# Kernel optimization log

Measured on AMD Instinct MI355X. Metric: run time of the kernel, lower is better.

Reference implementation:

```python
import jax, jax.numpy as jnp
import numpy as np

EPS = 1e-5


def conv3d(x, w, b, stride, pad, groups):
    # x: [B,C,D,H,W], w: [O, C//groups, kd, kh, kw]
    out = jax.lax.conv_general_dilated(
        x, w, (stride, stride, stride), [(pad, pad)] * 3,
        dimension_numbers=("NCDHW", "OIDHW", "NCDHW"),
        feature_group_count=groups)
    return out + b[None, :, None, None, None]


def setup_inputs() -> dict:
    key = jax.random.key(0)
    ks = jax.random.split(key, 8)
    B, N, C, h = 4, 4096, 256, 8
    s = lambda k, shp, sc=0.02: jax.random.normal(k, shp, jnp.float32) * sc
    return {
        "x": jax.random.normal(ks[0], (B, N, C), jnp.float32),
        "q_dw_w": s(ks[1], (C, 1, 3, 3, 3)), "q_dw_b": jnp.zeros((C,), jnp.float32),
        "bn_gamma": jnp.ones((C,), jnp.float32), "bn_beta": jnp.zeros((C,), jnp.float32),
        "bn_mean": jnp.zeros((C,), jnp.float32), "bn_var": jnp.ones((C,), jnp.float32),
        "q_pw_w": s(ks[2], (C, C)), "q_pw_b": jnp.zeros((C,), jnp.float32),
        "sr_w": s(ks[3], (C, 1, 3, 3, 3)), "sr_b": jnp.zeros((C,), jnp.float32),
        "ln_gamma": jnp.ones((C,), jnp.float32), "ln_beta": jnp.zeros((C,), jnp.float32),
        "kv_w": s(ks[4], (2 * C, C)),
        "trans_w": s(ks[5], (h, h), 0.3), "trans_b": jnp.zeros((h,), jnp.float32),
        "proj_w": s(ks[6], (C, C)), "proj_b": jnp.zeros((C,), jnp.float32),
        "H": 16, "W": 16, "L": 16,
    }


def reference(x, q_dw_w, q_dw_b, bn_gamma, bn_beta, bn_mean, bn_var,
              q_pw_w, q_pw_b, sr_w, sr_b, ln_gamma, ln_beta, kv_w,
              trans_w, trans_b, proj_w, proj_b, H, W, L):
    B, N, C = x.shape
    h = trans_w.shape[0]
    d = C // h
    scale = d ** -0.5

    # [B,N,C] -> [B,C,H,W,L] (N split row-major into H,W,L)
    xq = x.reshape(B, H, W, L, C).transpose(0, 4, 1, 2, 3)

    # --- q path: SepConv3d = depthwise conv -> BatchNorm (inference) -> pointwise ---
    q = conv3d(xq, q_dw_w, q_dw_b, 1, 1, C)
    q = (q - bn_mean[None, :, None, None, None]) * (
        bn_gamma / jnp.sqrt(bn_var + EPS))[None, :, None, None, None] \
        + bn_beta[None, :, None, None, None]
    q = jnp.einsum("oc,bcxyz->boxyz", q_pw_w, q) + q_pw_b[None, :, None, None, None]
    # 'b (h d) l w k -> b h (lwk) d'
    q = q.reshape(B, h, d, N).transpose(0, 1, 3, 2)  # [B,h,N,d]

    # --- sr path: strided depthwise conv -> LayerNorm -> kv Linear ---
    xs = conv3d(xq, sr_w, sr_b, 2, 1, C)           # [B,C,H/2,W/2,L/2]
    M = xs.shape[2] * xs.shape[3] * xs.shape[4]
    xs = xs.reshape(B, C, M).transpose(0, 2, 1)     # [B,M,C]
    mu = xs.mean(-1, keepdims=True)
    var = xs.var(-1, keepdims=True)
    xs = (xs - mu) / jnp.sqrt(var + EPS) * ln_gamma + ln_beta
    kv = xs @ kv_w.T                                # [B,M,2C]
    kv = kv.reshape(B, M, 2, h, d).transpose(2, 0, 3, 1, 4)
    k, v = kv[0], kv[1]                             # [B,h,M,d]

    # --- attention with per-head 1x1 conv transform + InstanceNorm ---
    attn = jnp.einsum("bhnd,bhmd->bhnm", q, k) * scale      # [B,h,N,M]
    attn = jnp.einsum("ij,bjnm->binm", trans_w, attn) + trans_b[None, :, None, None]
    attn = jax.nn.softmax(attn, axis=-1)
    m2 = attn.mean((2, 3), keepdims=True)
    v2 = attn.var((2, 3), keepdims=True)
    attn = (attn - m2) / jnp.sqrt(v2 + EPS)

    out = jnp.einsum("bhnm,bhmd->bhnd", attn, v)
    out = out.transpose(0, 2, 1, 3).reshape(B, N, C)
    out = out @ proj_w.T + proj_b
    return out
```

## Files before the change

kernel.cpp:

```cpp
#include <hip/hip_runtime.h>
#include <hip/hip_bf16.h>

#define SCALE_QK 0.17677669529663687f

__global__ __launch_bounds__(256) void prep_kernel(
    const float* __restrict__ pw, const float* __restrict__ kvw,
    const float* __restrict__ pjw,
    float* __restrict__ wtpw, float* __restrict__ wtkv, float* __restrict__ wtpj,
    float* __restrict__ ssq, float* __restrict__ sumv) {
  const int g = blockIdx.x * 256 + threadIdx.x;
  if (g < 65536) {
    const int c = g >> 8, o = g & 255;
    wtpw[g] = pw[o * 256 + c];
  } else if (g < 196608) {
    const int g2 = g - 65536;
    const int c = g2 >> 9, o = g2 & 511;
    wtkv[g2] = kvw[o * 256 + c];
  } else {
    const int g3 = g - 196608;
    const int c = g3 >> 8, o = g3 & 255;
    wtpj[g3] = pjw[o * 256 + c];
  }
  if (g < 512) ssq[g] = 0.0f;
  if (g >= 512 && g < 512 + 1024) sumv[g - 512] = 0.0f;
}

__global__ __launch_bounds__(256) void dwbn_kernel(
    const float* __restrict__ x, const float* __restrict__ w,
    const float* __restrict__ wb, const float* __restrict__ bg,
    const float* __restrict__ bb, const float* __restrict__ bm,
    const float* __restrict__ bv, float* __restrict__ outq) {
  const int blk = blockIdx.x;
  const int b = blk >> 12, n = blk & 4095;
  const int i0 = n >> 8, i1 = (n >> 4) & 15, i2 = n & 15;
  const int c = threadIdx.x;
  float acc = wb[c];
#pragma unroll
  for (int k0 = 0; k0 < 3; ++k0) {
    const int z = i0 + k0 - 1;
    if ((unsigned)z >= 16u) continue;
#pragma unroll
    for (int k1 = 0; k1 < 3; ++k1) {
      const int y = i1 + k1 - 1;
      if ((unsigned)y >= 16u) continue;
#pragma unroll
      for (int k2 = 0; k2 < 3; ++k2) {
        const int xx = i2 + k2 - 1;
        if ((unsigned)xx >= 16u) continue;
        acc = fmaf(w[c * 27 + (k0 * 3 + k1) * 3 + k2],
                   x[((b * 4096) + ((z * 16 + y) * 16 + xx)) * 256 + c], acc);
      }
    }
  }
  const float sc = bg[c] * rsqrtf(bv[c] + 1e-5f);
  outq[blk * 256 + c] = (acc - bm[c]) * sc + bb[c];
}

__global__ __launch_bounds__(256) void srln_kernel(
    const float* __restrict__ x, const float* __restrict__ w,
    const float* __restrict__ wb, const float* __restrict__ lg,
    const float* __restrict__ lb, float* __restrict__ outx) {
  const int blk = blockIdx.x;
  const int b = blk >> 9, m = blk & 511;
  const int o0 = m >> 6, o1 = (m >> 3) & 7, o2 = m & 7;
  const int c = threadIdx.x;
  float acc = wb[c];
#pragma unroll
  for (int k0 = 0; k0 < 3; ++k0) {
    const int z = o0 * 2 + k0 - 1;
    if ((unsigned)z >= 16u) continue;
#pragma unroll
    for (int k1 = 0; k1 < 3; ++k1) {
      const int y = o1 * 2 + k1 - 1;
      if ((unsigned)y >= 16u) continue;
#pragma unroll
      for (int k2 = 0; k2 < 3; ++k2) {
        const int xx = o2 * 2 + k2 - 1;
        if ((unsigned)xx >= 16u) continue;
        acc = fmaf(w[c * 27 + (k0 * 3 + k1) * 3 + k2],
                   x[((b * 4096) + ((z * 16 + y) * 16 + xx)) * 256 + c], acc);
      }
    }
  }
  __shared__ float r1[4], r2[4];
  float s1 = acc, s2 = acc * acc;
#pragma unroll
  for (int off = 32; off >= 1; off >>= 1) {
    s1 += __shfl_xor(s1, off);
    s2 += __shfl_xor(s2, off);
  }
  const int t = threadIdx.x;
  if ((t & 63) == 0) { r1[t >> 6] = s1; r2[t >> 6] = s2; }
  __syncthreads();
  const float mu = (r1[0] + r1[1] + r1[2] + r1[3]) * (1.0f / 256.0f);
  const float ms = (r2[0] + r2[1] + r2[2] + r2[3]) * (1.0f / 256.0f);
  const float rs = rsqrtf(ms - mu * mu + 1e-5f);
  outx[blk * 256 + c] = (acc - mu) * rs * lg[c] + lb[c];
}

template <int MODE>
__global__ __launch_bounds__(256) void gemm_kernel(
    const float* __restrict__ A, const float* __restrict__ Wt,
    const float* __restrict__ bias, float* __restrict__ Out, const int ldW,
    const float* __restrict__ sumv, const float* __restrict__ rstd) {
  __shared__ float a_t[32][68];
  __shared__ float w_s[32][132];
  const int t = threadIdx.x;
  const int r0 = blockIdx.x * 64;
  const int c0 = blockIdx.y * 128;
  const int rt = t & 15, ct = t >> 4;
  const int bidx = r0 >> 12;
  const float invM = 1.0f / 512.0f;
  float acc[4][8];
#pragma unroll
  for (int rr = 0; rr < 4; ++rr)
#pragma unroll
    for (int cc = 0; cc < 8; ++cc) acc[rr][cc] = 0.0f;

  for (int k0 = 0; k0 < 256; k0 += 32) {
    {
      const int kk = t & 31;
      int rl = t >> 5;
#pragma unroll
      for (int p = 0; p < 8; ++p, rl += 8) {
        float v = A[(r0 + rl) * 256 + k0 + kk];
        if (MODE == 1) {
          const int kg = k0 + kk;
          v = (v - invM * sumv[bidx * 256 + kg]) * rstd[bidx * 8 + (kg >> 5)];
        }
        a_t[kk][rl] = v;
      }
    }
    {
      const int cq = (t & 31) * 4;
      int kk = t >> 5;
#pragma unroll
      for (int p = 0; p < 4; ++p, kk += 8) {
        const float4 v = *(const float4*)&Wt[(k0 + kk) * ldW + c0 + cq];
        *(float4*)&w_s[kk][cq] = v;
      }
    }
    __syncthreads();
#pragma unroll
    for (int kk = 0; kk < 32; ++kk) {
      const float4 a4 = *(const float4*)&a_t[kk][rt * 4];
      const float av[4] = {a4.x, a4.y, a4.z, a4.w};
      float4 w4[2];
#pragma unroll
      for (int q = 0; q < 2; ++q) w4[q] = *(const float4*)&w_s[kk][ct * 8 + q * 4];
#pragma unroll
      for (int rr = 0; rr < 4; ++rr) {
#pragma unroll
        for (int q = 0; q < 2; ++q) {
          acc[rr][q * 4 + 0] = fmaf(av[rr], w4[q].x, acc[rr][q * 4 + 0]);
          acc[rr][q * 4 + 1] = fmaf(av[rr], w4[q].y, acc[rr][q * 4 + 1]);
          acc[rr][q * 4 + 2] = fmaf(av[rr], w4[q].z, acc[rr][q * 4 + 2]);
          acc[rr][q * 4 + 3] = fmaf(av[rr], w4[q].w, acc[rr][q * 4 + 3]);
        }
      }
    }
    __syncthreads();
  }
#pragma unroll
  for (int rr = 0; rr < 4; ++rr) {
    const int row = r0 + rt * 4 + rr;
#pragma unroll
    for (int q = 0; q < 2; ++q) {
      const int cc = c0 + ct * 8 + q * 4;
      float4 o;
      o.x = acc[rr][q * 4 + 0];
      o.y = acc[rr][q * 4 + 1];
      o.z = acc[rr][q * 4 + 2];
      o.w = acc[rr][q * 4 + 3];
      if (bias != nullptr) {
        o.x += bias[cc + 0]; o.y += bias[cc + 1];
        o.z += bias[cc + 2]; o.w += bias[cc + 3];
      }
      *(float4*)&Out[row * ldW + cc] = o;
    }
  }
}

__global__ __launch_bounds__(256) void kt_kernel(const float* __restrict__ kvb,
                                                 float* __restrict__ ktb) {
  __shared__ float tile[32][33];
  const int blk = blockIdx.x;
  const int b = blk >> 7, mt = (blk >> 3) & 15, k8 = blk & 7;
  const int m0 = mt * 32, k0 = k8 * 32;
  const int t = threadIdx.x;
  {
    const int ml = t >> 3, kl = (t & 7) * 4;
    const float4 v = *(const float4*)&kvb[((b * 512 + m0 + ml) * 512) + k0 + kl];
    tile[ml][kl + 0] = v.x; tile[ml][kl + 1] = v.y;
    tile[ml][kl + 2] = v.z; tile[ml][kl + 3] = v.w;
  }
  __syncthreads();
  {
    const int kl = t >> 3, ml = (t & 7) * 4;
    float4 o;
    o.x = tile[ml + 0][kl]; o.y = tile[ml + 1][kl];
    o.z = tile[ml + 2][kl]; o.w = tile[ml + 3][kl];
    *(float4*)&ktb[((b * 256 + k0 + kl) * 512) + m0 + ml] = o;
  }
}

__global__ __launch_bounds__(256) void sumv_kernel(const float* __restrict__ kvb,
                                                   float* __restrict__ sumv) {
  const int blk = blockIdx.x;
  const int b = blk >> 3, grp = blk & 7;
  const int c = threadIdx.x;
  float s = 0.0f;
  for (int mm = 0; mm < 64; ++mm) {
    const int m = grp * 64 + mm;
    s += kvb[((b * 512 + m) * 512) + 256 + c];
  }
  atomicAdd(&sumv[b * 256 + c], s);
}

__global__ void rstd_kernel(const float* __restrict__ ssq, float* __restrict__ rstd) {
  const int t = threadIdx.x;
  if (t < 32) {
    float s = 0.0f;
#pragma unroll
    for (int sp = 0; sp < 16; ++sp) s += ssq[sp * 32 + t];
    const float e2 = s * (1.0f / (4096.0f * 512.0f));
    const float invM = 1.0f / 512.0f;
    rstd[t] = rsqrtf(e2 - invM * invM + 1e-5f);
  }
}

__device__ __forceinline__ int pswz2(int row, int m) {
  const int q = m >> 2;
  const int qs = q ^ ((q >> 3) & 7);
  return row * 512 + (qs << 2) + (m & 3);
}

__global__ __launch_bounds__(512, 4) void attn_kernel(
    const float* __restrict__ qb, const float* __restrict__ ktb,
    const float* __restrict__ kvb, const float* __restrict__ tw,
    float* __restrict__ ssq, float* __restrict__ out_un) {
  __shared__ float P[16384];
  __shared__ float Qs[8 * 256];
  __shared__ float sq_lds[8][8];
  const int t = threadIdx.x;
  const int blk = blockIdx.x;
  const int b = blk >> 9;
  const int n0 = (blk & 511) << 3;
  const int w = t >> 6, l = t & 63;

  {
    const int row = t >> 6, kq = t & 63;
    const float4 v = *(const float4*)&qb[((b * 4096 + n0 + row) * 256) + kq * 4];
    float4 s;
    s.x = v.x * SCALE_QK; s.y = v.y * SCALE_QK;
    s.z = v.z * SCALE_QK; s.w = v.w * SCALE_QK;
    *(float4*)&Qs[row * 256 + kq * 4] = s;
  }
  __syncthreads();

  float acc[8][8];
#pragma unroll
  for (int r = 0; r < 8; ++r)
#pragma unroll
    for (int e = 0; e < 8; ++e) acc[r][e] = 0.0f;
  {
    const float* ktr = &ktb[(size_t)((b * 256 + w * 32) << 9)];
    const int m2 = l * 2;
#pragma unroll 4
    for (int k = 0; k < 32; ++k) {
      const float2 c0 = *(const float2*)&ktr[(k << 9) + m2];
      const float2 c1 = *(const float2*)&ktr[(k << 9) + 128 + m2];
      const float2 c2 = *(const float2*)&ktr[(k << 9) + 256 + m2];
      const float2 c3 = *(const float2*)&ktr[(k << 9) + 384 + m2];
#pragma unroll
      for (int r = 0; r < 8; ++r) {
        const float qv = Qs[r * 256 + w * 32 + k];
        acc[r][0] = fmaf(qv, c0.x, acc[r][0]); acc[r][1] = fmaf(qv, c0.y, acc[r][1]);
        acc[r][2] = fmaf(qv, c1.x, acc[r][2]); acc[r][3] = fmaf(qv, c1.y, acc[r][3]);
        acc[r][4] = fmaf(qv, c2.x, acc[r][4]); acc[r][5] = fmaf(qv, c2.y, acc[r][5]);
        acc[r][6] = fmaf(qv, c3.x, acc[r][6]); acc[r][7] = fmaf(qv, c3.y, acc[r][7]);
      }
    }
  }

  float Wr[8][8];
#pragma unroll
  for (int i = 0; i < 8; ++i)
#pragma unroll
    for (int jj = 0; jj < 8; ++jj) Wr[i][jj] = tw[i * 8 + jj];

  float mixed[8][8];
#pragma unroll
  for (int i = 0; i < 8; ++i)
#pragma unroll
    for (int e = 0; e < 8; ++e) mixed[i][e] = 0.0f;

#pragma unroll
  for (int r = 0; r < 8; ++r) {
    float2 s0; s0.x = acc[r][0]; s0.y = acc[r][1];
    float2 s1; s1.x = acc[r][2]; s1.y = acc[r][3];
    *(float2*)&P[(r * 8 + w) * 256 + l * 2] = s0;
    *(float2*)&P[(r * 8 + w) * 256 + 128 + l * 2] = s1;
  }
  __syncthreads();
#pragma unroll
  for (int jj = 0; jj < 8; ++jj) {
    const float2 ra = *(const float2*)&P[(w * 8 + jj) * 256 + l * 2];
    const float2 rb = *(const float2*)&P[(w * 8 + jj) * 256 + 128 + l * 2];
#pragma unroll
    for (int i = 0; i < 8; ++i) {
      mixed[i][0] = fmaf(Wr[i][jj], ra.x, mixed[i][0]);
      mixed[i][1] = fmaf(Wr[i][jj], ra.y, mixed[i][1]);
      mixed[i][2] = fmaf(Wr[i][jj], rb.x, mixed[i][2]);
      mixed[i][3] = fmaf(Wr[i][jj], rb.y, mixed[i][3]);
    }
  }
  __syncthreads();
#pragma unroll
  for (int r = 0; r < 8; ++r) {
    float2 s0; s0.x = acc[r][4]; s0.y = acc[r][5];
    float2 s1; s1.x = acc[r][6]; s1.y = acc[r][7];
    *(float2*)&P[(r * 8 + w) * 256 + l * 2] = s0;
    *(float2*)&P[(r * 8 + w) * 256 + 128 + l * 2] = s1;
  }
  __syncthreads();
#pragma unroll
  for (int jj = 0; jj < 8; ++jj) {
    const float2 ra = *(const float2*)&P[(w * 8 + jj) * 256 + l * 2];
    const float2 rb = *(const float2*)&P[(w * 8 + jj) * 256 + 128 + l * 2];
#pragma unroll
    for (int i = 0; i < 8; ++i) {
      mixed[i][4] = fmaf(Wr[i][jj], ra.x, mixed[i][4]);
      mixed[i][5] = fmaf(Wr[i][jj], ra.y, mixed[i][5]);
      mixed[i][6] = fmaf(Wr[i][jj], rb.x, mixed[i][6]);
      mixed[i][7] = fmaf(Wr[i][jj], rb.y, mixed[i][7]);
    }
  }
  __syncthreads();

#pragma unroll
  for (int i = 0; i < 8; ++i) {
    float mx = mixed[i][0];
#pragma unroll
    for (int e = 1; e < 8; ++e) mx = fmaxf(mx, mixed[i][e]);
#pragma unroll
    for (int off = 32; off >= 1; off >>= 1) mx = fmaxf(mx, __shfl_xor(mx, off));
    float s = 0.0f;
#pragma unroll
    for (int e = 0; e < 8; ++e) {
      const float ev = __expf(mixed[i][e] - mx);
      mixed[i][e] = ev;
      s += ev;
    }
#pragma unroll
    for (int off = 32; off >= 1; off >>= 1) s += __shfl_xor(s, off);
    const float rinv = 1.0f / s;
    float sq = 0.0f;
#pragma unroll
    for (int e = 0; e < 8; ++e) {
      const float p = mixed[i][e] * rinv;
      mixed[i][e] = p;
      sq = fmaf(p, p, sq);
    }
#pragma unroll
    for (int off = 32; off >= 1; off >>= 1) sq += __shfl_xor(sq, off);
    if (l == 0) sq_lds[w][i] = sq;
  }
  __syncthreads();
  if (t < 8) {
    float s8 = 0.0f;
#pragma unroll
    for (int r = 0; r < 8; ++r) s8 += sq_lds[r][t];
    atomicAdd(&ssq[(blk & 15) * 32 + b * 8 + t], s8);
  }

  const int il = w & 3, mh = w >> 2;
  const int mgrp = l >> 3, dl = l & 7;

#pragma unroll
  for (int i = 0; i < 4; ++i) {
#pragma unroll
    for (int e = 0; e < 4; ++e) {
      float2 pv;
      pv.x = mixed[i][e * 2 + 0];
      pv.y = mixed[i][e * 2 + 1];
      *(float2*)&P[pswz2(w * 4 + i, e * 128 + l * 2)] = pv;
    }
  }
  __syncthreads();
  {
    float av[8][4];
#pragma unroll
    for (int r = 0; r < 8; ++r)
#pragma unroll
      for (int e = 0; e < 4; ++e) av[r][e] = 0.0f;
    const int mb = mh * 256 + mgrp * 32;
    const int vcol = 256 + il * 32 + dl * 4;
#pragma unroll 2
    for (int mq = 0; mq < 8; ++mq) {
      const int m0 = mb + mq * 4;
      float4 p4[8];
#pragma unroll
      for (int r = 0; r < 8; ++r) p4[r] = *(const float4*)&P[pswz2(r * 4 + il, m0)];
#pragma unroll
      for (int e = 0; e < 4; ++e) {
        const float4 v4 = *(const float4*)&kvb[((b * 512 + m0 + e) * 512) + vcol];
#pragma unroll
        for (int r = 0; r < 8; ++r) {
          const float p = (&p4[r].x)[e];
          av[r][0] = fmaf(p, v4.x, av[r][0]);
          av[r][1] = fmaf(p, v4.y, av[r][1]);
          av[r][2] = fmaf(p, v4.z, av[r][2]);
          av[r][3] = fmaf(p, v4.w, av[r][3]);
        }
      }
    }
#pragma unroll
    for (int r = 0; r < 8; ++r)
#pragma unroll
      for (int e = 0; e < 4; ++e) {
        float v = av[r][e];
        v += __shfl_xor(v, 8);
        v += __shfl_xor(v, 16);
        v += __shfl_xor(v, 32);
        av[r][e] = v;
      }
    __syncthreads();
    if (l < 8) {
#pragma unroll
      for (int r = 0; r < 8; ++r) {
        float4 o;
        o.x = av[r][0]; o.y = av[r][1]; o.z = av[r][2]; o.w = av[r][3];
        *(float4*)&P[w * 256 + r * 32 + dl * 4] = o;
      }
    }
  }
  __syncthreads();
#pragma unroll
  for (int rep = 0; rep < 2; ++rep) {
    const int idx = rep * 512 + t;
    const int il2 = idx >> 8, r2i = (idx >> 5) & 7, dd = idx & 31;
    const float s = P[il2 * 256 + r2i * 32 + dd] + P[(il2 + 4) * 256 + r2i * 32 + dd];
    out_un[((b * 4096) + n0 + r2i) * 256 + il2 * 32 + dd] = s;
  }
  __syncthreads();

#pragma unroll
  for (int i = 0; i < 4; ++i) {
#pragma unroll
    for (int e = 0; e < 4; ++e) {
      float2 pv;
      pv.x = mixed[4 + i][e * 2 + 0];
      pv.y = mixed[4 + i][e * 2 + 1];
      *(float2*)&P[pswz2(w * 4 + i, e * 128 + l * 2)] = pv;
    }
  }
  __syncthreads();
  {
    float av[8][4];
#pragma unroll
    for (int r = 0; r < 8; ++r)
#pragma unroll
      for (int e = 0; e < 4; ++e) av[r][e] = 0.0f;
    const int mb = mh * 256 + mgrp * 32;
    const int vcol = 256 + (4 + il) * 32 + dl * 4;
#pragma unroll 2
    for (int mq = 0; mq < 8; ++mq) {
      const int m0 = mb + mq * 4;
      float4 p4[8];
#pragma unroll
      for (int r = 0; r < 8; ++r) p4[r] = *(const float4*)&P[pswz2(r * 4 + il, m0)];
#pragma unroll
      for (int e = 0; e < 4; ++e) {
        const float4 v4 = *(const float4*)&kvb[((b * 512 + m0 + e) * 512) + vcol];
#pragma unroll
        for (int r = 0; r < 8; ++r) {
          const float p = (&p4[r].x)[e];
          av[r][0] = fmaf(p, v4.x, av[r][0]);
          av[r][1] = fmaf(p, v4.y, av[r][1]);
          av[r][2] = fmaf(p, v4.z, av[r][2]);
          av[r][3] = fmaf(p, v4.w, av[r][3]);
        }
      }
    }
#pragma unroll
    for (int r = 0; r < 8; ++r)
#pragma unroll
      for (int e = 0; e < 4; ++e) {
        float v = av[r][e];
        v += __shfl_xor(v, 8);
        v += __shfl_xor(v, 16);
        v += __shfl_xor(v, 32);
        av[r][e] = v;
      }
    __syncthreads();
    if (l < 8) {
#pragma unroll
      for (int r = 0; r < 8; ++r) {
        float4 o;
        o.x = av[r][0]; o.y = av[r][1]; o.z = av[r][2]; o.w = av[r][3];
        *(float4*)&P[w * 256 + r * 32 + dl * 4] = o;
      }
    }
  }
  __syncthreads();
#pragma unroll
  for (int rep = 0; rep < 2; ++rep) {
    const int idx = rep * 512 + t;
    const int il2 = idx >> 8, r2i = (idx >> 5) & 7, dd = idx & 31;
    const float s = P[il2 * 256 + r2i * 32 + dd] + P[(il2 + 4) * 256 + r2i * 32 + dd];
    out_un[((b * 4096) + n0 + r2i) * 256 + (4 + il2) * 32 + dd] = s;
  }
}

extern "C" void kernel_launch(void* const* d_in, const int* in_sizes, int n_in,
                              void* d_out, int out_size, void* d_ws, size_t ws_size,
                              hipStream_t stream) {
  const float* x   = (const float*)d_in[0];
  const float* qdww= (const float*)d_in[1];
  const float* qdwb= (const float*)d_in[2];
  const float* bng = (const float*)d_in[3];
  const float* bnb = (const float*)d_in[4];
  const float* bnm = (const float*)d_in[5];
  const float* bnv = (const float*)d_in[6];
  const float* pw  = (const float*)d_in[7];
  const float* pwb = (const float*)d_in[8];
  const float* srw = (const float*)d_in[9];
  const float* srb = (const float*)d_in[10];
  const float* lng = (const float*)d_in[11];
  const float* lnb = (const float*)d_in[12];
  const float* kvw = (const float*)d_in[13];
  const float* tw  = (const float*)d_in[14];
  const float* pjw = (const float*)d_in[16];
  const float* pjb = (const float*)d_in[17];
  float* out = (float*)d_out;
  float* ws = (float*)d_ws;

  float* qdw   = ws + 0;
  float* qbuf  = ws + 4194304;
  float* xsln  = ws + 8388608;
  float* kvb   = ws + 8912896;
  float* ktb   = ws + 9961472;
  float* wtpw  = ws + 10485760;
  float* wtkv  = ws + 10551296;
  float* wtpj  = ws + 10682368;
  float* sumvp = ws + 10747904;
  float* ssqp  = ws + 10748928;
  float* rstdp = ws + 10749440;

  prep_kernel<<<1024, 256, 0, stream>>>(pw, kvw, pjw, wtpw, wtkv, wtpj, ssqp, sumvp);
  dwbn_kernel<<<16384, 256, 0, stream>>>(x, qdww, qdwb, bng, bnb, bnm, bnv, qdw);
  gemm_kernel<0><<<dim3(256, 2), 256, 0, stream>>>(qdw, wtpw, pwb, qbuf, 256, nullptr, nullptr);
  srln_kernel<<<2048, 256, 0, stream>>>(x, srw, srb, lng, lnb, xsln);
  gemm_kernel<0><<<dim3(32, 4), 256, 0, stream>>>(xsln, wtkv, nullptr, kvb, 512, nullptr, nullptr);
  kt_kernel<<<512, 256, 0, stream>>>(kvb, ktb);
  sumv_kernel<<<32, 256, 0, stream>>>(kvb, sumvp);
  attn_kernel<<<2048, 512, 0, stream>>>(qbuf, ktb, kvb, tw, ssqp, out);
  rstd_kernel<<<1, 64, 0, stream>>>(ssqp, rstdp);
  gemm_kernel<1><<<dim3(256, 2), 256, 0, stream>>>(out, wtpj, pjb, out, 256, sumvp, rstdp);
}
```

Baseline: 470.6 us.

## Compute QK scores with split-bf16 MFMA and fold head-mix into Q

```diff
diff --git a/kernel.cpp b/kernel.cpp
--- a/kernel.cpp
+++ b/kernel.cpp
@@ -2,6 +2,18 @@
 #include <hip/hip_bf16.h>
 
 #define SCALE_QK 0.17677669529663687f
+
+typedef __attribute__((ext_vector_type(8))) short bf16x8;
+typedef __attribute__((ext_vector_type(4))) float f32x4;
+
+__device__ __forceinline__ unsigned short bf16_rne(float v) {
+  const unsigned int b = __float_as_uint(v);
+  const unsigned int r = b + 0x7FFFu + ((b >> 16) & 1u);
+  return (unsigned short)(r >> 16);
+}
+__device__ __forceinline__ float bf16_f32(unsigned short h) {
+  return __uint_as_float(((unsigned int)h) << 16);
+}
 
 __global__ __launch_bounds__(256) void prep_kernel(
     const float* __restrict__ pw, const float* __restrict__ kvw,
@@ -182,7 +194,7 @@
 }
 
 __global__ __launch_bounds__(256) void kt_kernel(const float* __restrict__ kvb,
-                                                 float* __restrict__ ktb) {
+                                                 unsigned short* __restrict__ kthl) {
   __shared__ float tile[32][33];
   const int blk = blockIdx.x;
   const int b = blk >> 7, mt = (blk >> 3) & 15, k8 = blk & 7;
@@ -196,11 +208,27 @@
   }
   __syncthreads();
   {
-    const int kl = t >> 3, ml = (t & 7) * 4;
-    float4 o;
-    o.x = tile[ml + 0][kl]; o.y = tile[ml + 1][kl];
-    o.z = tile[ml + 2][kl]; o.w = tile[ml + 3][kl];
-    *(float4*)&ktb[((b * 256 + k0 + kl) * 512) + m0 + ml] = o;
+    const int s = t >> 7, kt8l = (t >> 5) & 3, mloc = t & 31;
+    unsigned int pk[4];
+#pragma unroll
+    for (int ep = 0; ep < 4; ++ep) {
+      unsigned short h0, h1;
+      {
+        const float v = tile[mloc][kt8l * 8 + ep * 2];
+        const unsigned short hi = bf16_rne(v);
+        h0 = (s == 0) ? hi : bf16_rne(v - bf16_f32(hi));
+      }
+      {
+        const float v = tile[mloc][kt8l * 8 + ep * 2 + 1];
+        const unsigned short hi = bf16_rne(v);
+        h1 = (s == 0) ? hi : bf16_rne(v - bf16_f32(hi));
+      }
+      pk[ep] = (unsigned int)h0 | ((unsigned int)h1 << 16);
+    }
+    const int kt8 = k8 * 4 + kt8l;
+    uint4 u;
+    u.x = pk[0]; u.y = pk[1]; u.z = pk[2]; u.w = pk[3];
+    *(uint4*)&kthl[((((size_t)b * 32 + kt8) * 512 + (m0 + mloc)) * 2 + s) * 8] = u;
   }
 }
 
@@ -236,141 +264,149 @@
 }
 
 __global__ __launch_bounds__(512, 4) void attn_kernel(
-    const float* __restrict__ qb, const float* __restrict__ ktb,
+    const float* __restrict__ qb, const unsigned short* __restrict__ kthl,
     const float* __restrict__ kvb, const float* __restrict__ tw,
     float* __restrict__ ssq, float* __restrict__ out_un) {
   __shared__ float P[16384];
-  __shared__ float Qs[8 * 256];
-  __shared__ float sq_lds[8][8];
-  const int t = threadIdx.x;
-  const int blk = blockIdx.x;
-  const int b = blk >> 9;
-  const int n0 = (blk & 511) << 3;
+  __shared__ float red[64][8][2];
+  __shared__ float red2[64][2];
+  __shared__ float sq_lds[64][8];
+  const int t = threadIdx.x, blk = blockIdx.x;
+  const int b = blk >> 9, n0 = (blk & 511) << 3;
   const int w = t >> 6, l = t & 63;
+  const int l15 = l & 15, l4 = l >> 4;
+  unsigned short* Au = (unsigned short*)P;
 
   {
-    const int row = t >> 6, kq = t & 63;
-    const float4 v = *(const float4*)&qb[((b * 4096 + n0 + row) * 256) + kq * 4];
-    float4 s;
-    s.x = v.x * SCALE_QK; s.y = v.y * SCALE_QK;
-    s.z = v.z * SCALE_QK; s.w = v.w * SCALE_QK;
-    *(float4*)&Qs[row * 256 + kq * 4] = s;
-  }
-  __syncthreads();
-
-  float acc[8][8];
-#pragma unroll
-  for (int r = 0; r < 8; ++r)
-#pragma unroll
-    for (int e = 0; e < 8; ++e) acc[r][e] = 0.0f;
-  {
-    const float* ktr = &ktb[(size_t)((b * 256 + w * 32) << 9)];
-    const int m2 = l * 2;
-#pragma unroll 4
-    for (int k = 0; k < 32; ++k) {
-      const float2 c0 = *(const float2*)&ktr[(k << 9) + m2];
-      const float2 c1 = *(const float2*)&ktr[(k << 9) + 128 + m2];
-      const float2 c2 = *(const float2*)&ktr[(k << 9) + 256 + m2];
-      const float2 c3 = *(const float2*)&ktr[(k << 9) + 384 + m2];
-#pragma unroll
-      for (int r = 0; r < 8; ++r) {
-        const float qv = Qs[r * 256 + w * 32 + k];
-        acc[r][0] = fmaf(qv, c0.x, acc[r][0]); acc[r][1] = fmaf(qv, c0.y, acc[r][1]);
-        acc[r][2] = fmaf(qv, c1.x, acc[r][2]); acc[r][3] = fmaf(qv, c1.y, acc[r][3]);
-        acc[r][4] = fmaf(qv, c2.x, acc[r][4]); acc[r][5] = fmaf(qv, c2.y, acc[r][5]);
-        acc[r][6] = fmaf(qv, c3.x, acc[r][6]); acc[r][7] = fmaf(qv, c3.y, acc[r][7]);
-      }
-    }
-  }
-
-  float Wr[8][8];
-#pragma unroll
-  for (int i = 0; i < 8; ++i)
-#pragma unroll
-    for (int jj = 0; jj < 8; ++jj) Wr[i][jj] = tw[i * 8 + jj];
-
-  float mixed[8][8];
-#pragma unroll
-  for (int i = 0; i < 8; ++i)
-#pragma unroll
-    for (int e = 0; e < 8; ++e) mixed[i][e] = 0.0f;
-
-#pragma unroll
-  for (int r = 0; r < 8; ++r) {
-    float2 s0; s0.x = acc[r][0]; s0.y = acc[r][1];
-    float2 s1; s1.x = acc[r][2]; s1.y = acc[r][3];
-    *(float2*)&P[(r * 8 + w) * 256 + l * 2] = s0;
-    *(float2*)&P[(r * 8 + w) * 256 + 128 + l * 2] = s1;
-  }
-  __syncthreads();
-#pragma unroll
-  for (int jj = 0; jj < 8; ++jj) {
-    const float2 ra = *(const float2*)&P[(w * 8 + jj) * 256 + l * 2];
-    const float2 rb = *(const float2*)&P[(w * 8 + jj) * 256 + 128 + l * 2];
+    const int r = t >> 6, c4 = (t & 63) * 4;
+    const float4 q4 = *(const float4*)&qb[((b * 4096 + n0 + r) * 256) + c4];
+    const float qv[4] = {q4.x, q4.y, q4.z, q4.w};
+    const int kt = c4 >> 5;
 #pragma unroll
     for (int i = 0; i < 8; ++i) {
-      mixed[i][0] = fmaf(Wr[i][jj], ra.x, mixed[i][0]);
-      mixed[i][1] = fmaf(Wr[i][jj], ra.y, mixed[i][1]);
-      mixed[i][2] = fmaf(Wr[i][jj], rb.x, mixed[i][2]);
-      mixed[i][3] = fmaf(Wr[i][jj], rb.y, mixed[i][3]);
-    }
-  }
-  __syncthreads();
-#pragma unroll
-  for (int r = 0; r < 8; ++r) {
-    float2 s0; s0.x = acc[r][4]; s0.y = acc[r][5];
-    float2 s1; s1.x = acc[r][6]; s1.y = acc[r][7];
-    *(float2*)&P[(r * 8 + w) * 256 + l * 2] = s0;
-    *(float2*)&P[(r * 8 + w) * 256 + 128 + l * 2] = s1;
-  }
-  __syncthreads();
-#pragma unroll
-  for (int jj = 0; jj < 8; ++jj) {
-    const float2 ra = *(const float2*)&P[(w * 8 + jj) * 256 + l * 2];
-    const float2 rb = *(const float2*)&P[(w * 8 + jj) * 256 + 128 + l * 2];
-#pragma unroll
-    for (int i = 0; i < 8; ++i) {
-      mixed[i][4] = fmaf(Wr[i][jj], ra.x, mixed[i][4]);
-      mixed[i][5] = fmaf(Wr[i][jj], ra.y, mixed[i][5]);
-      mixed[i][6] = fmaf(Wr[i][jj], rb.x, mixed[i][6]);
-      mixed[i][7] = fmaf(Wr[i][jj], rb.y, mixed[i][7]);
-    }
-  }
-  __syncthreads();
-
-#pragma unroll
-  for (int i = 0; i < 8; ++i) {
-    float mx = mixed[i][0];
-#pragma unroll
-    for (int e = 1; e < 8; ++e) mx = fmaxf(mx, mixed[i][e]);
-#pragma unroll
-    for (int off = 32; off >= 1; off >>= 1) mx = fmaxf(mx, __shfl_xor(mx, off));
-    float s = 0.0f;
-#pragma unroll
-    for (int e = 0; e < 8; ++e) {
-      const float ev = __expf(mixed[i][e] - mx);
-      mixed[i][e] = ev;
-      s += ev;
-    }
-#pragma unroll
-    for (int off = 32; off >= 1; off >>= 1) s += __shfl_xor(s, off);
-    const float rinv = 1.0f / s;
-    float sq = 0.0f;
-#pragma unroll
-    for (int e = 0; e < 8; ++e) {
-      const float p = mixed[i][e] * rinv;
-      mixed[i][e] = p;
-      sq = fmaf(p, p, sq);
-    }
-#pragma unroll
-    for (int off = 32; off >= 1; off >>= 1) sq += __shfl_xor(sq, off);
-    if (l == 0) sq_lds[w][i] = sq;
+      const float wij = tw[i * 8 + kt] * SCALE_QK;
+      const int mt = i >> 1;
+      const int rowin = (i & 1) * 8 + r;
+#pragma unroll
+      for (int cc = 0; cc < 4; ++cc) {
+        const int c = c4 + cc;
+        const float v = qv[cc] * wij;
+        const unsigned short hi = bf16_rne(v);
+        const unsigned short lo = bf16_rne(v - bf16_f32(hi));
+        const int lane = rowin | (((c & 31) >> 3) << 4);
+        const int idx = (((mt * 8 + kt) * 2) * 64 + lane) * 8 + (c & 7);
+        Au[idx] = hi;
+        Au[idx + 512] = lo;
+      }
+    }
+  }
+  __syncthreads();
+
+  f32x4 C[4][4];
+#pragma unroll
+  for (int mt = 0; mt < 4; ++mt)
+#pragma unroll
+    for (int tt = 0; tt < 4; ++tt) C[mt][tt] = (f32x4){0.f, 0.f, 0.f, 0.f};
+
+#pragma unroll
+  for (int kt = 0; kt < 8; ++kt) {
+#pragma unroll
+    for (int th = 0; th < 2; ++th) {
+      bf16x8 Bh[2], Bl[2];
+#pragma unroll
+      for (int tp = 0; tp < 2; ++tp) {
+        const int m = w * 64 + (th * 2 + tp) * 16 + l15;
+        const size_t bi = ((((size_t)b * 32 + kt * 4 + l4) * 512 + m) * 2) * 8;
+        Bh[tp] = *(const bf16x8*)&kthl[bi];
+        Bl[tp] = *(const bf16x8*)&kthl[bi + 8];
+      }
+#pragma unroll
+      for (int mt = 0; mt < 4; ++mt) {
+        const int ab = (((mt * 8 + kt) * 2) * 64 + l) * 8;
+        const bf16x8 Ah = *(const bf16x8*)&Au[ab];
+        const bf16x8 Al = *(const bf16x8*)&Au[ab + 512];
+#pragma unroll
+        for (int tp = 0; tp < 2; ++tp) {
+          const int ti = th * 2 + tp;
+          C[mt][ti] = __builtin_amdgcn_mfma_f32_16x16x32_bf16(Ah, Bh[tp], C[mt][ti], 0, 0, 0);
+          C[mt][ti] = __builtin_amdgcn_mfma_f32_16x16x32_bf16(Ah, Bl[tp], C[mt][ti], 0, 0, 0);
+          C[mt][ti] = __builtin_amdgcn_mfma_f32_16x16x32_bf16(Al, Bh[tp], C[mt][ti], 0, 0, 0);
+        }
+      }
+    }
+  }
+
+  float mxloc[4][4];
+#pragma unroll
+  for (int mt = 0; mt < 4; ++mt) {
+#pragma unroll
+    for (int rg = 0; rg < 4; ++rg) {
+      float mx = fmaxf(fmaxf(C[mt][0][rg], C[mt][1][rg]),
+                       fmaxf(C[mt][2][rg], C[mt][3][rg]));
+      mx = fmaxf(mx, __shfl_xor(mx, 1));
+      mx = fmaxf(mx, __shfl_xor(mx, 2));
+      mx = fmaxf(mx, __shfl_xor(mx, 4));
+      mx = fmaxf(mx, __shfl_xor(mx, 8));
+      mxloc[mt][rg] = mx;
+      float s = 0.f;
+#pragma unroll
+      for (int tt = 0; tt < 4; ++tt) {
+        const float e = __expf(C[mt][tt][rg] - mx);
+        C[mt][tt][rg] = e;
+        s += e;
+      }
+      s += __shfl_xor(s, 1);
+      s += __shfl_xor(s, 2);
+      s += __shfl_xor(s, 4);
+      s += __shfl_xor(s, 8);
+      if (l15 == 0) {
+        const int row = mt * 16 + l4 * 4 + rg;
+        red[row][w][0] = mx;
+        red[row][w][1] = s;
+      }
+    }
+  }
+  __syncthreads();
+  if (t < 64) {
+    float MX = -3.4e38f;
+#pragma unroll
+    for (int w8 = 0; w8 < 8; ++w8) MX = fmaxf(MX, red[t][w8][0]);
+    float S = 0.f;
+#pragma unroll
+    for (int w8 = 0; w8 < 8; ++w8) S += red[t][w8][1] * __expf(red[t][w8][0] - MX);
+    red2[t][0] = MX;
+    red2[t][1] = 1.0f / S;
+  }
+  __syncthreads();
+
+#pragma unroll
+  for (int mt = 0; mt < 4; ++mt) {
+#pragma unroll
+    for (int rg = 0; rg < 4; ++rg) {
+      const int row = mt * 16 + l4 * 4 + rg;
+      const float2 g2 = *(const float2*)&red2[row][0];
+      const float factor = __expf(mxloc[mt][rg] - g2.x) * g2.y;
+      float sq = 0.f;
+#pragma unroll
+      for (int tt = 0; tt < 4; ++tt) {
+        const float p = C[mt][tt][rg] * factor;
+        C[mt][tt][rg] = p;
+        sq = fmaf(p, p, sq);
+      }
+      sq += __shfl_xor(sq, 1);
+      sq += __shfl_xor(sq, 2);
+      sq += __shfl_xor(sq, 4);
+      sq += __shfl_xor(sq, 8);
+      if (l15 == 0) sq_lds[row][w] = sq;
+    }
   }
   __syncthreads();
   if (t < 8) {
-    float s8 = 0.0f;
-#pragma unroll
-    for (int r = 0; r < 8; ++r) s8 += sq_lds[r][t];
+    float s8 = 0.f;
+#pragma unroll
+    for (int rr = 0; rr < 8; ++rr)
+#pragma unroll
+      for (int w8 = 0; w8 < 8; ++w8) s8 += sq_lds[t * 8 + rr][w8];
     atomicAdd(&ssq[(blk & 15) * 32 + b * 8 + t], s8);
   }
 
@@ -378,13 +414,16 @@
   const int mgrp = l >> 3, dl = l & 7;
 
 #pragma unroll
-  for (int i = 0; i < 4; ++i) {
-#pragma unroll
-    for (int e = 0; e < 4; ++e) {
-      float2 pv;
-      pv.x = mixed[i][e * 2 + 0];
-      pv.y = mixed[i][e * 2 + 1];
-      *(float2*)&P[pswz2(w * 4 + i, e * 128 + l * 2)] = pv;
+  for (int mt = 0; mt < 2; ++mt) {
+#pragma unroll
+    for (int tt = 0; tt < 4; ++tt) {
+#pragma unroll
+      for (int rg = 0; rg < 4; ++rg) {
+        const int row64 = mt * 16 + l4 * 4 + rg;
+        const int hd_ = row64 >> 3, r_ = row64 & 7;
+        const int m = w * 64 + tt * 16 + l15;
+        P[pswz2(r_ * 4 + hd_, m)] = C[mt][tt][rg];
+      }
     }
   }
   __syncthreads();
@@ -446,13 +485,16 @@
   __syncthreads();
 
 #pragma unroll
-  for (int i = 0; i < 4; ++i) {
-#pragma unroll
-    for (int e = 0; e < 4; ++e) {
-      float2 pv;
-      pv.x = mixed[4 + i][e * 2 + 0];
-      pv.y = mixed[4 + i][e * 2 + 1];
-      *(float2*)&P[pswz2(w * 4 + i, e * 128 + l * 2)] = pv;
+  for (int mt = 0; mt < 2; ++mt) {
+#pragma unroll
+    for (int tt = 0; tt < 4; ++tt) {
+#pragma unroll
+      for (int rg = 0; rg < 4; ++rg) {
+        const int row64 = (mt + 2) * 16 + l4 * 4 + rg;
+        const int hd_ = (row64 >> 3) - 4, r_ = row64 & 7;
+        const int m = w * 64 + tt * 16 + l15;
+        P[pswz2(r_ * 4 + hd_, m)] = C[mt + 2][tt][rg];
+      }
     }
   }
   __syncthreads();
@@ -540,7 +582,7 @@
   float* qbuf  = ws + 4194304;
   float* xsln  = ws + 8388608;
   float* kvb   = ws + 8912896;
-  float* ktb   = ws + 9961472;
+  unsigned short* kthl = (unsigned short*)(ws + 9961472);
   float* wtpw  = ws + 10485760;
   float* wtkv  = ws + 10551296;
   float* wtpj  = ws + 10682368;
@@ -553,9 +595,9 @@
   gemm_kernel<0><<<dim3(256, 2), 256, 0, stream>>>(qdw, wtpw, pwb, qbuf, 256, nullptr, nullptr);
   srln_kernel<<<2048, 256, 0, stream>>>(x, srw, srb, lng, lnb, xsln);
   gemm_kernel<0><<<dim3(32, 4), 256, 0, stream>>>(xsln, wtkv, nullptr, kvb, 512, nullptr, nullptr);
-  kt_kernel<<<512, 256, 0, stream>>>(kvb, ktb);
+  kt_kernel<<<512, 256, 0, stream>>>(kvb, kthl);
   sumv_kernel<<<32, 256, 0, stream>>>(kvb, sumvp);
-  attn_kernel<<<2048, 512, 0, stream>>>(qbuf, ktb, kvb, tw, ssqp, out);
+  attn_kernel<<<2048, 512, 0, stream>>>(qbuf, kthl, kvb, tw, ssqp, out);
   rstd_kernel<<<1, 64, 0, stream>>>(ssqp, rstdp);
   gemm_kernel<1><<<dim3(256, 2), 256, 0, stream>>>(out, wtpj, pjb, out, 256, sumvp, rstdp);
 }
```

New measurement: 491.2 us. 4.4% more time.
